# Kernel tuning notes

Measured on AMD Instinct MI355X. Metric: run time of the kernel, lower is better.

## Reference

```python
import jax, jax.numpy as jnp
import numpy as np

NUM_SLICE = 32


def setup_inputs() -> dict:
    key = jax.random.key(0)
    k1, k2 = jax.random.split(key)
    B, C, N = 8, 128, 65536
    inp = jax.random.normal(k1, (B, C, N, 1), dtype=jnp.float32)
    slice_idx_mat = jax.random.randint(k2, (B, N), 0, NUM_SLICE, dtype=jnp.int32)
    return {"input": inp, "slice_idx_mat": slice_idx_mat}


def reference(input, slice_idx_mat) -> jnp.ndarray:
    # Slice max-pool: for each (batch, channel, slice), max over points whose
    # slice index equals that slice. The original CUDA kernel initializes the
    # output to 0, so the result is clamped at >= 0 (empty slices -> 0).
    B, C, N, _ = input.shape
    S = NUM_SLICE
    # [B, N, C] flattened to [B*N, C] so one segment_max covers all batches.
    x = jnp.transpose(input[..., 0], (0, 2, 1)).reshape(B * N, C)
    seg = (slice_idx_mat + jnp.arange(B, dtype=slice_idx_mat.dtype)[:, None] * S).reshape(B * N)
    pooled = jax.ops.segment_max(x, seg, num_segments=B * S)  # [B*S, C]
    pooled = jnp.maximum(pooled, jnp.float32(0.0))  # init-to-zero semantics
    out = jnp.transpose(pooled.reshape(B, S, C), (0, 2, 1))[..., None]  # [B,C,S,1]
    return out
```

## Files before the change

### kernel.cpp

```cpp
#include <hip/hip_runtime.h>

#define NUM_SLICE 32

constexpr int Bc = 8;
constexpr int Cc = 128;
constexpr int Nc = 65536;

constexpr int CPB     = 2;
constexpr int CHUNK   = 16384;
constexpr int THREADS = 256;
constexpr int PTS_PER_ITER = THREADS * 4;
constexpr int NITER   = CHUNK / PTS_PER_ITER;
constexpr int ACC_LD  = 33;
constexpr int NREP    = 2;

typedef float f32x4 __attribute__((ext_vector_type(4)));
typedef int   i32x4 __attribute__((ext_vector_type(4)));

__global__ __launch_bounds__(THREADS) void init_out_kernel(float* out, int n) {
    int i = blockIdx.x * blockDim.x + threadIdx.x;
    if (i < n) out[i] = 0.0f;
}

__global__ __launch_bounds__(THREADS) void slice_pool_kernel(
    const float* __restrict__ in,
    const int*   __restrict__ idx,
    unsigned int* __restrict__ out)
{
    __shared__ unsigned int acc[NREP][CPB * ACC_LD];

    const int t = threadIdx.x;
    for (int i = t; i < NREP * CPB * ACC_LD; i += THREADS)
        (&acc[0][0])[i] = 0u;
    __syncthreads();

    const int chunk = blockIdx.x;
    const int cg    = blockIdx.y;
    const int b     = blockIdx.z;
    const int c0    = cg * CPB;
    const int n0    = chunk * CHUNK;
    const int rep   = t & 1;

    const i32x4* __restrict__ idx4   = (const i32x4*)(idx + (size_t)b * Nc + n0);
    const float* __restrict__ inbase = in + ((size_t)b * Cc + c0) * Nc + n0;

    unsigned int* __restrict__ accr = acc[rep];

    #pragma unroll 2
    for (int p = 0; p < NITER; ++p) {
        const int e    = p * THREADS + t;
        const i32x4 iv = idx4[e];
        const int off  = e * 4;
        #pragma unroll
        for (int c = 0; c < CPB; ++c) {
            const f32x4 v = *(const f32x4*)(inbase + (size_t)c * Nc + off);
            const int base = c * ACC_LD;
            const unsigned int bx = __float_as_uint(fmaxf(v[0], 0.0f));
            const unsigned int by = __float_as_uint(fmaxf(v[1], 0.0f));
            const unsigned int bz = __float_as_uint(fmaxf(v[2], 0.0f));
            const unsigned int bw = __float_as_uint(fmaxf(v[3], 0.0f));
            if (bx) atomicMax(&accr[base + iv[0]], bx);
            if (by) atomicMax(&accr[base + iv[1]], by);
            if (bz) atomicMax(&accr[base + iv[2]], bz);
            if (bw) atomicMax(&accr[base + iv[3]], bw);
        }
    }
    __syncthreads();

    if (t < CPB * NUM_SLICE) {
        const int c = t >> 5;
        const int s = t & 31;
        unsigned int v = acc[0][c * ACC_LD + s];
        const unsigned int v1 = acc[1][c * ACC_LD + s];
        v = v > v1 ? v : v1;
        if (v != 0u) {
            atomicMax(&out[(((size_t)b * Cc) + c0 + c) * NUM_SLICE + s], v);
        }
    }
}

extern "C" void kernel_launch(void* const* d_in, const int* in_sizes, int n_in,
                              void* d_out, int out_size, void* d_ws, size_t ws_size,
                              hipStream_t stream) {
    const float* in  = (const float*)d_in[0];
    const int*   idx = (const int*)  d_in[1];
    float* out = (float*)d_out;

    const int n_out = Bc * Cc * NUM_SLICE;
    init_out_kernel<<<(n_out + THREADS - 1) / THREADS, THREADS, 0, stream>>>(out, n_out);

    dim3 grid(Nc / CHUNK, Cc / CPB, Bc);
    slice_pool_kernel<<<grid, THREADS, 0, stream>>>(in, idx, (unsigned int*)out);
}
```

Measured before the change: 49.67 us.

## Process full point range per block and drop init kernel and global atomics

Each block now covers all N points for its channel pair with 1024 threads instead of splitting N into four chunks. The output is written directly with plain stores, so the separate zero-init kernel and the global atomicMax merge go away. The cost is fewer blocks (512 instead of 2048) and more threads contending on the same small LDS accumulator, which may increase shared-atomic contention and reduce latency hiding.

Measured after the change: 45.82 us (median of 2 runs). -7.8%, faster.

```diff
diff --git a/kernel.cpp b/kernel.cpp
--- a/kernel.cpp
+++ b/kernel.cpp
@@ -7,22 +7,16 @@
 constexpr int Nc = 65536;
 
 constexpr int CPB     = 2;
-constexpr int CHUNK   = 16384;
-constexpr int THREADS = 256;
+constexpr int THREADS = 1024;
 constexpr int PTS_PER_ITER = THREADS * 4;
-constexpr int NITER   = CHUNK / PTS_PER_ITER;
+constexpr int NITER   = Nc / PTS_PER_ITER;
 constexpr int ACC_LD  = 33;
 constexpr int NREP    = 2;
 
 typedef float f32x4 __attribute__((ext_vector_type(4)));
 typedef int   i32x4 __attribute__((ext_vector_type(4)));
 
-__global__ __launch_bounds__(THREADS) void init_out_kernel(float* out, int n) {
-    int i = blockIdx.x * blockDim.x + threadIdx.x;
-    if (i < n) out[i] = 0.0f;
-}
-
-__global__ __launch_bounds__(THREADS) void slice_pool_kernel(
+__global__ __launch_bounds__(THREADS, 8) void slice_pool_kernel(
     const float* __restrict__ in,
     const int*   __restrict__ idx,
     unsigned int* __restrict__ out)
@@ -30,19 +24,16 @@
     __shared__ unsigned int acc[NREP][CPB * ACC_LD];
 
     const int t = threadIdx.x;
-    for (int i = t; i < NREP * CPB * ACC_LD; i += THREADS)
-        (&acc[0][0])[i] = 0u;
+    if (t < NREP * CPB * ACC_LD) (&acc[0][0])[t] = 0u;
     __syncthreads();
 
-    const int chunk = blockIdx.x;
-    const int cg    = blockIdx.y;
-    const int b     = blockIdx.z;
-    const int c0    = cg * CPB;
-    const int n0    = chunk * CHUNK;
-    const int rep   = t & 1;
+    const int cg = blockIdx.x;
+    const int b  = blockIdx.y;
+    const int c0 = cg * CPB;
+    const int rep = t & 1;
 
-    const i32x4* __restrict__ idx4   = (const i32x4*)(idx + (size_t)b * Nc + n0);
-    const float* __restrict__ inbase = in + ((size_t)b * Cc + c0) * Nc + n0;
+    const i32x4* __restrict__ idx4   = (const i32x4*)(idx + (size_t)b * Nc);
+    const float* __restrict__ inbase = in + ((size_t)b * Cc + c0) * Nc;
 
     unsigned int* __restrict__ accr = acc[rep];
 
@@ -73,9 +64,7 @@
         unsigned int v = acc[0][c * ACC_LD + s];
         const unsigned int v1 = acc[1][c * ACC_LD + s];
         v = v > v1 ? v : v1;
-        if (v != 0u) {
-            atomicMax(&out[(((size_t)b * Cc) + c0 + c) * NUM_SLICE + s], v);
-        }
+        out[(((size_t)b * Cc) + c0 + c) * NUM_SLICE + s] = v;
     }
 }
 
@@ -84,11 +73,8 @@
                               hipStream_t stream) {
     const float* in  = (const float*)d_in[0];
     const int*   idx = (const int*)  d_in[1];
-    float* out = (float*)d_out;
+    unsigned int* out = (unsigned int*)d_out;
 
-    const int n_out = Bc * Cc * NUM_SLICE;
-    init_out_kernel<<<(n_out + THREADS - 1) / THREADS, THREADS, 0, stream>>>(out, n_out);
-
-    dim3 grid(Nc / CHUNK, Cc / CPB, Bc);
-    slice_pool_kernel<<<grid, THREADS, 0, stream>>>(in, idx, (unsigned int*)out);
+    dim3 grid(Cc / CPB, Bc);
+    slice_pool_kernel<<<grid, THREADS, 0, stream>>>(in, idx, out);
 }
```
